# Performance work log

Measured on AMD Instinct MI355X. Metric: run time of the kernel, lower is better.

The kernel has to match this reference:

```python
import jax, jax.numpy as jnp
import numpy as np

EMBED_DIM = 1024
HEAD_SIZE = 256
B, T = 8, 2048


def setup_inputs() -> dict:
    key = jax.random.key(0)
    kx, kq, kk, kv = jax.random.split(key, 4)
    x = jax.random.normal(kx, (B, T, EMBED_DIM), dtype=jnp.float32)
    # torch Linear(E, H, bias=False): weight [H, E], y = x @ W.T; store as [E, H]
    s = 1.0 / np.sqrt(EMBED_DIM)
    Wq = jax.random.uniform(kq, (EMBED_DIM, HEAD_SIZE), jnp.float32, -s, s)
    Wk = jax.random.uniform(kk, (EMBED_DIM, HEAD_SIZE), jnp.float32, -s, s)
    Wv = jax.random.uniform(kv, (EMBED_DIM, HEAD_SIZE), jnp.float32, -s, s)
    return {"x": x, "Wq": Wq, "Wk": Wk, "Wv": Wv}


def reference(x, Wq, Wk, Wv):
    # x: [B, T, E]
    q = jnp.einsum("bte,eh->bth", x, Wq)
    k = jnp.einsum("bte,eh->bth", x, Wk)
    v = jnp.einsum("bte,eh->bth", x, Wv)
    scale = HEAD_SIZE ** -0.5
    scores = jnp.einsum("bth,bsh->bts", q, k) * scale  # [B, T, T]
    t = x.shape[1]
    causal = jnp.tril(jnp.ones((t, t), dtype=bool))
    scores = jnp.where(causal, scores, -jnp.inf)
    attn = jax.nn.softmax(scores, axis=-1)  # dropout p=0.0 -> identity
    return jnp.einsum("bts,bsh->bth", attn, v)
```

## Files before the change

kernel.cpp:

```cpp
#include <hip/hip_runtime.h>
#include <stdint.h>

#define EMBED 1024
#define HEAD  256
#define BATCH 8
#define SEQ   2048
#define NTOK  (BATCH*SEQ)

typedef __attribute__((ext_vector_type(8)))  short  s16x8;
typedef __attribute__((ext_vector_type(4)))  float  f32x4;
typedef __attribute__((ext_vector_type(16))) float  f32x16;
typedef __attribute__((ext_vector_type(4)))  unsigned short u16x4;

__device__ __forceinline__ unsigned short f2bf(float f) {
  union { float f; uint32_t u; } v; v.f = f;
  return (unsigned short)((v.u + 0x7FFFu + ((v.u >> 16) & 1u)) >> 16);
}

__device__ __forceinline__ uint32_t cvtpk(float a, float b) {
  uint32_t r;
  asm("v_cvt_pk_bf16_f32 %0, %1, %2" : "=v"(r) : "v"(a), "v"(b));
  return r;
}

__device__ __forceinline__ void gload_lds16(const void* g, void* l) {
  __builtin_amdgcn_global_load_lds((const __attribute__((address_space(1))) void*)g,
                                   (__attribute__((address_space(3))) void*)l, 16, 0, 0);
}

__global__ __launch_bounds__(256) void wt_kernel(const float* __restrict__ Wq,
                                                 const float* __restrict__ Wk,
                                                 const float* __restrict__ Wv,
                                                 unsigned short* __restrict__ Wt) {
  int idx = blockIdx.x * 256 + threadIdx.x;
  int e  = idx & (EMBED - 1);
  int hw = idx >> 10;
  int w  = hw >> 8;
  int h  = hw & 255;
  const float* W = (w == 0) ? Wq : (w == 1) ? Wk : Wv;
  float sc = (w == 0) ? 0.0625f : 1.0f;
  Wt[idx] = f2bf(W[(size_t)e * HEAD + h] * sc);
}

__global__ __launch_bounds__(256) void xprep_kernel(const float* __restrict__ x,
                                                    unsigned short* __restrict__ xb) {
  size_t i8 = ((size_t)blockIdx.x * 256 + threadIdx.x) * 8;
  f32x4 f0 = *(const f32x4*)(x + i8);
  f32x4 f1 = *(const f32x4*)(x + i8 + 4);
  u16x4 p0, p1;
  #pragma unroll
  for (int j = 0; j < 4; j++) { p0[j] = f2bf(f0[j]); p1[j] = f2bf(f1[j]); }
  *(u16x4*)(xb + i8)     = p0;
  *(u16x4*)(xb + i8 + 4) = p1;
}

__global__ __launch_bounds__(256) void proj_kernel(const unsigned short* __restrict__ xb,
    const unsigned short* __restrict__ Wt,
    unsigned short* __restrict__ qo, unsigned short* __restrict__ ko,
    unsigned short* __restrict__ vfrag) {
  __shared__ unsigned short Al[128 * 64];
  __shared__ unsigned short Bl[128 * 64];
  const int tid  = threadIdx.x;
  const int lane = tid & 63;
  const int wid  = tid >> 6;
  const int wm = wid >> 1, wn = wid & 1;
  const int bid  = blockIdx.x;
  const int xcd  = bid & 7;
  const int i6   = bid >> 3;
  const int mloc = i6 & 15;
  const int nz   = i6 >> 4;
  const int m0 = (xcd * 16 + mloc) * 128;
  const int n0 = (nz & 1) * 128;
  const int w  = nz >> 1;
  const unsigned short* Wtw = Wt + (size_t)w * 256 * EMBED;

  f32x4 acc[4][4] = {};

  for (int k0 = 0; k0 < EMBED; k0 += 64) {
    #pragma unroll
    for (int i = 0; i < 4; i++) {
      int u = tid + 256 * i;
      int row = u >> 3, sc = u & 7;
      int scs = sc ^ (row & 7);
      gload_lds16(xb + (size_t)(m0 + row) * EMBED + k0 + scs * 8,
                  &Al[i * 2048 + wid * 512]);
    }
    #pragma unroll
    for (int i = 0; i < 4; i++) {
      int u = tid + 256 * i;
      int row = u >> 3, sc = u & 7;
      int scs = sc ^ (row & 7);
      gload_lds16(Wtw + (size_t)(n0 + row) * EMBED + k0 + scs * 8,
                  &Bl[i * 2048 + wid * 512]);
    }
    __syncthreads();
    #pragma unroll
    for (int kk = 0; kk < 2; kk++) {
      s16x8 a[4], bfr[4];
      #pragma unroll
      for (int mi = 0; mi < 4; mi++) {
        int row = wm * 64 + mi * 16 + (lane & 15);
        int c = (4 * kk + (lane >> 4)) ^ (row & 7);
        a[mi] = *(const s16x8*)(&Al[row * 64 + c * 8]);
      }
      #pragma unroll
      for (int ni = 0; ni < 4; ni++) {
        int row = wn * 64 + ni * 16 + (lane & 15);
        int c = (4 * kk + (lane >> 4)) ^ (row & 7);
        bfr[ni] = *(const s16x8*)(&Bl[row * 64 + c * 8]);
      }
      #pragma unroll
      for (int mi = 0; mi < 4; mi++)
        #pragma unroll
        for (int ni = 0; ni < 4; ni++)
          acc[mi][ni] = __builtin_amdgcn_mfma_f32_16x16x32_bf16(a[mi], bfr[ni], acc[mi][ni], 0, 0, 0);
    }
    __syncthreads();
  }

  if (w < 2) {
    unsigned short* dst = (w == 0) ? qo : ko;
    #pragma unroll
    for (int mi = 0; mi < 4; mi++)
      #pragma unroll
      for (int r = 0; r < 4; r++) {
        int mrow = m0 + wm * 64 + mi * 16 + 4 * (lane >> 4) + r;
        #pragma unroll
        for (int ni = 0; ni < 4; ni++) {
          int col = n0 + wn * 64 + ni * 16 + (lane & 15);
          dst[(size_t)mrow * HEAD + col] = f2bf(acc[mi][ni][r]);
        }
      }
  } else {
    #pragma unroll
    for (int mi = 0; mi < 4; mi++) {
      int base = m0 + wm * 64 + mi * 16 + 4 * (lane >> 4);
      int toko = base & 31;
      size_t vb0 = (size_t)(base >> 11) * 524288
                 + (size_t)((base & 2047) >> 5) * 8192
                 + ((toko >> 4) & 1) * 512 + ((toko >> 3) & 1) * 256 + (toko & 7);
      #pragma unroll
      for (int ni = 0; ni < 4; ni++) {
        int col = n0 + wn * 64 + ni * 16 + (lane & 15);
        u16x4 pk;
        #pragma unroll
        for (int r = 0; r < 4; r++) pk[r] = f2bf(acc[mi][ni][r]);
        *(u16x4*)(vfrag + vb0 + (size_t)(col >> 5) * 1024 + (col & 31) * 8) = pk;
      }
    }
  }
}

__global__ __launch_bounds__(256, 1) void attn_kernel(const unsigned short* __restrict__ qb,
    const unsigned short* __restrict__ kb, const unsigned short* __restrict__ vfrag,
    float* __restrict__ out) {
  __shared__ unsigned short Kl[4][32 * 256];
  __shared__ float mls[4][2][32];
  const int tid  = threadIdx.x;
  const int lane = tid & 63;
  const int w    = tid >> 6;
  const int hi   = lane >> 5;
  const int q    = lane & 31;
  const int bid  = blockIdx.x;
  const int b = bid & 7;
  const int t = 63 - (bid >> 3);
  const unsigned short* qB = qb + (size_t)b * SEQ * HEAD;
  const unsigned short* kB = kb + (size_t)b * SEQ * HEAD;
  const unsigned short* vfB = vfrag + (size_t)b * 524288;
  float* outB = out + (size_t)b * SEQ * HEAD;
  const int qg = t * 32 + q;

  s16x8 qf[16];
  #pragma unroll
  for (int s = 0; s < 16; s++)
    qf[s] = *(const s16x8*)(qB + (size_t)qg * HEAD + s * 16 + hi * 8);

  f32x16 o[8] = {};
  float m = -1e30f, lsum = 0.f;

  const int nt = t + 1;
  const int cl = (nt + 3) >> 2;
  const int j0 = w * cl;
  const int j1 = (j0 + cl < nt) ? (j0 + cl) : nt;
  unsigned short* Kw = (unsigned short*)Kl[w];

  for (int j = j0; j < j1; j++) {
    #pragma unroll
    for (int i = 0; i < 16; i++) {
      int cl_ = i * 64 + lane;
      int key = cl_ >> 5, c = cl_ & 31;
      gload_lds16(kB + (size_t)(j * 32 + key) * HEAD + (size_t)((c ^ (key & 15)) * 8),
                  &Kw[i * 512]);
    }
    asm volatile("s_waitcnt vmcnt(0)" ::: "memory");
    __builtin_amdgcn_sched_barrier(0);
    f32x16 s0 = {}, s1 = {};
    #pragma unroll
    for (int s = 0; s < 8; s++) {
      s16x8 kf = *(const s16x8*)((const char*)Kw +
                   (q * 512 + (((2 * s + hi) ^ (q & 15)) << 4)));
      s0 = __builtin_amdgcn_mfma_f32_32x32x16_bf16(kf, qf[s], s0, 0, 0, 0);
    }
    #pragma unroll
    for (int s = 8; s < 16; s++) {
      s16x8 kf = *(const s16x8*)((const char*)Kw +
                   (q * 512 + (((2 * s + hi) ^ (q & 15)) << 4)));
      s1 = __builtin_amdgcn_mfma_f32_32x32x16_bf16(kf, qf[s], s1, 0, 0, 0);
    }
    f32x16 sv;
    #pragma unroll
    for (int r = 0; r < 16; r++) sv[r] = s0[r] + s1[r];
    if (j == t) {
      #pragma unroll
      for (int r = 0; r < 16; r++) {
        int kg = j * 32 + (r & 3) + 8 * (r >> 2) + 4 * hi;
        sv[r] = (kg > qg) ? -1e30f : sv[r];
      }
    }
    float mt = sv[0];
    #pragma unroll
    for (int r = 1; r < 16; r++) mt = fmaxf(mt, sv[r]);
    mt = fmaxf(mt, __shfl_xor(mt, 32));
    float mn = fmaxf(m, mt);
    if (!__all(mt - m <= 8.0f)) {
      float al = __expf(m - mn);
      lsum *= al;
      #pragma unroll
      for (int ht = 0; ht < 8; ht++)
        #pragma unroll
        for (int r = 0; r < 16; r++) o[ht][r] *= al;
      m = mn;
    }
    #pragma unroll
    for (int r = 0; r < 16; r++) sv[r] = __expf(sv[r] - m);
    float rs = 0.f;
    #pragma unroll
    for (int r = 0; r < 16; r++) rs += sv[r];
    rs += __shfl_xor(rs, 32);
    lsum += rs;
    uint32_t cc[8], dd[8];
    #pragma unroll
    for (int i = 0; i < 8; i++) cc[i] = cvtpk(sv[2 * i], sv[2 * i + 1]);
    #pragma unroll
    for (int i = 0; i < 8; i++) dd[i] = (uint32_t)__shfl_xor((int)cc[i], 32);
    union { s16x8 v; uint32_t u[4]; } pf0, pf1;
    pf0.u[0] = hi ? dd[2] : cc[0];
    pf0.u[1] = hi ? dd[3] : cc[1];
    pf0.u[2] = hi ? cc[2] : dd[0];
    pf0.u[3] = hi ? cc[3] : dd[1];
    pf1.u[0] = hi ? dd[6] : cc[4];
    pf1.u[1] = hi ? dd[7] : cc[5];
    pf1.u[2] = hi ? cc[6] : dd[4];
    pf1.u[3] = hi ? cc[7] : dd[5];
    const unsigned short* vT = vfB + (size_t)j * 8192 + hi * 256 + q * 8;
    #pragma unroll
    for (int ht = 0; ht < 8; ht++) {
      s16x8 vf0 = *(const s16x8*)(vT + ht * 1024);
      o[ht] = __builtin_amdgcn_mfma_f32_32x32x16_bf16(vf0, pf0.v, o[ht], 0, 0, 0);
      s16x8 vf1 = *(const s16x8*)(vT + ht * 1024 + 512);
      o[ht] = __builtin_amdgcn_mfma_f32_32x32x16_bf16(vf1, pf1.v, o[ht], 0, 0, 0);
    }
  }

  __syncthreads();
  if (lane < 32) { mls[w][0][q] = m; mls[w][1][q] = lsum; }
  __syncthreads();
  float mx = mls[0][0][q];
  #pragma unroll
  for (int w2 = 1; w2 < 4; w2++) mx = fmaxf(mx, mls[w2][0][q]);
  float L = 0.f;
  #pragma unroll
  for (int w2 = 0; w2 < 4; w2++)
    L += __expf(mls[w2][0][q] - mx) * mls[w2][1][q];
  float aown = __expf(m - mx);
  #pragma unroll
  for (int ht = 0; ht < 8; ht++)
    #pragma unroll
    for (int r = 0; r < 16; r++) o[ht][r] *= aown;

  float* obuf = (float*)&Kl[0][0];
  for (int ph = 3; ph >= 0; ph--) {
    if (w == ph) {
      #pragma unroll
      for (int ht = 0; ht < 8; ht++)
        #pragma unroll
        for (int g2 = 0; g2 < 4; g2++) {
          int gp = 8 * ht + 2 * g2 + hi;
          float* ptr = &obuf[q * 256 + ((gp ^ (q & 15)) << 2)];
          f32x4 v4 = { o[ht][4*g2], o[ht][4*g2+1], o[ht][4*g2+2], o[ht][4*g2+3] };
          if (ph != 3) { f32x4 prev = *(f32x4*)ptr;
            #pragma unroll
            for (int z = 0; z < 4; z++) v4[z] += prev[z]; }
          if (ph != 0) { *(f32x4*)ptr = v4; }
          else {
            #pragma unroll
            for (int z = 0; z < 4; z++) v4[z] /= L;
            *(f32x4*)(outB + (size_t)qg * HEAD + ht * 32 + g2 * 8 + hi * 4) = v4;
          }
        }
    }
    __syncthreads();
  }
}

extern "C" void kernel_launch(void* const* d_in, const int* in_sizes, int n_in,
                              void* d_out, int out_size, void* d_ws, size_t ws_size,
                              hipStream_t stream) {
  const float* x  = (const float*)d_in[0];
  const float* Wq = (const float*)d_in[1];
  const float* Wk = (const float*)d_in[2];
  const float* Wv = (const float*)d_in[3];
  float* out = (float*)d_out;

  unsigned short* ws = (unsigned short*)d_ws;
  unsigned short* qb    = ws;
  unsigned short* kb    = qb + (size_t)NTOK * HEAD;
  unsigned short* vfrag = kb + (size_t)NTOK * HEAD;
  unsigned short* Wt    = vfrag + (size_t)NTOK * HEAD;
  unsigned short* xb    = Wt + (size_t)3 * HEAD * EMBED;

  hipLaunchKernelGGL(wt_kernel, dim3(3 * 256 * EMBED / 256), dim3(256), 0, stream,
                     Wq, Wk, Wv, Wt);
  hipLaunchKernelGGL(xprep_kernel, dim3(NTOK * EMBED / (256 * 8)), dim3(256), 0, stream,
                     x, xb);
  hipLaunchKernelGGL(proj_kernel, dim3(768), dim3(256), 0, stream,
                     xb, Wt, qb, kb, vfrag);
  hipLaunchKernelGGL(attn_kernel, dim3(512), dim3(256), 0, stream,
                     qb, kb, vfrag, out);
}
```

Before: 133.7 us.

## Double-buffer K tiles, pair causal query tiles per block, use exp2 softmax

Each attention block now handles two query tiles, a long one and a short one (t = 63-p and t = p). This balances causal work across 256 blocks instead of 512 uneven ones. K tiles are double-buffered in LDS, so the global-to-LDS load for the next tile overlaps compute on the current one. Softmax moves to exp2 by folding log2(e) into the Q weight scale, which removes a multiply per exponent. The cost is twice the LDS per block and more serialized work per block; 256 blocks may underfill the GPU's CUs.

Result: slower. 136.4 us (+2.0%).

```diff
diff --git a/kernel.cpp b/kernel.cpp
--- a/kernel.cpp
+++ b/kernel.cpp
@@ -38,7 +38,7 @@
   int w  = hw >> 8;
   int h  = hw & 255;
   const float* W = (w == 0) ? Wq : (w == 1) ? Wk : Wv;
-  float sc = (w == 0) ? 0.0625f : 1.0f;
+  float sc = (w == 0) ? 0.09016844f : 1.0f;
   Wt[idx] = f2bf(W[(size_t)e * HEAD + h] * sc);
 }
 
@@ -154,7 +154,7 @@
 __global__ __launch_bounds__(256, 1) void attn_kernel(const unsigned short* __restrict__ qb,
     const unsigned short* __restrict__ kb, const unsigned short* __restrict__ vfrag,
     float* __restrict__ out) {
-  __shared__ unsigned short Kl[4][32 * 256];
+  __shared__ unsigned short Kl[4][2][32 * 256];
   __shared__ float mls[4][2][32];
   const int tid  = threadIdx.x;
   const int lane = tid & 63;
@@ -163,144 +163,161 @@
   const int q    = lane & 31;
   const int bid  = blockIdx.x;
   const int b = bid & 7;
-  const int t = 63 - (bid >> 3);
+  const int p = bid >> 3;
   const unsigned short* qB = qb + (size_t)b * SEQ * HEAD;
   const unsigned short* kB = kb + (size_t)b * SEQ * HEAD;
   const unsigned short* vfB = vfrag + (size_t)b * 524288;
   float* outB = out + (size_t)b * SEQ * HEAD;
-  const int qg = t * 32 + q;
-
-  s16x8 qf[16];
-  #pragma unroll
-  for (int s = 0; s < 16; s++)
-    qf[s] = *(const s16x8*)(qB + (size_t)qg * HEAD + s * 16 + hi * 8);
-
-  f32x16 o[8] = {};
-  float m = -1e30f, lsum = 0.f;
-
-  const int nt = t + 1;
-  const int cl = (nt + 3) >> 2;
-  const int j0 = w * cl;
-  const int j1 = (j0 + cl < nt) ? (j0 + cl) : nt;
   unsigned short* Kw = (unsigned short*)Kl[w];
 
-  for (int j = j0; j < j1; j++) {
-    #pragma unroll
-    for (int i = 0; i < 16; i++) {
-      int cl_ = i * 64 + lane;
-      int key = cl_ >> 5, c = cl_ & 31;
-      gload_lds16(kB + (size_t)(j * 32 + key) * HEAD + (size_t)((c ^ (key & 15)) * 8),
-                  &Kw[i * 512]);
-    }
-    asm volatile("s_waitcnt vmcnt(0)" ::: "memory");
-    __builtin_amdgcn_sched_barrier(0);
-    f32x16 s0 = {}, s1 = {};
-    #pragma unroll
-    for (int s = 0; s < 8; s++) {
-      s16x8 kf = *(const s16x8*)((const char*)Kw +
-                   (q * 512 + (((2 * s + hi) ^ (q & 15)) << 4)));
-      s0 = __builtin_amdgcn_mfma_f32_32x32x16_bf16(kf, qf[s], s0, 0, 0, 0);
-    }
-    #pragma unroll
-    for (int s = 8; s < 16; s++) {
-      s16x8 kf = *(const s16x8*)((const char*)Kw +
-                   (q * 512 + (((2 * s + hi) ^ (q & 15)) << 4)));
-      s1 = __builtin_amdgcn_mfma_f32_32x32x16_bf16(kf, qf[s], s1, 0, 0, 0);
-    }
-    f32x16 sv;
-    #pragma unroll
-    for (int r = 0; r < 16; r++) sv[r] = s0[r] + s1[r];
-    if (j == t) {
-      #pragma unroll
-      for (int r = 0; r < 16; r++) {
-        int kg = j * 32 + (r & 3) + 8 * (r >> 2) + 4 * hi;
-        sv[r] = (kg > qg) ? -1e30f : sv[r];
-      }
-    }
-    float mt = sv[0];
-    #pragma unroll
-    for (int r = 1; r < 16; r++) mt = fmaxf(mt, sv[r]);
-    mt = fmaxf(mt, __shfl_xor(mt, 32));
-    float mn = fmaxf(m, mt);
-    if (!__all(mt - m <= 8.0f)) {
-      float al = __expf(m - mn);
-      lsum *= al;
-      #pragma unroll
-      for (int ht = 0; ht < 8; ht++)
-        #pragma unroll
-        for (int r = 0; r < 16; r++) o[ht][r] *= al;
-      m = mn;
-    }
-    #pragma unroll
-    for (int r = 0; r < 16; r++) sv[r] = __expf(sv[r] - m);
-    float rs = 0.f;
-    #pragma unroll
-    for (int r = 0; r < 16; r++) rs += sv[r];
-    rs += __shfl_xor(rs, 32);
-    lsum += rs;
-    uint32_t cc[8], dd[8];
-    #pragma unroll
-    for (int i = 0; i < 8; i++) cc[i] = cvtpk(sv[2 * i], sv[2 * i + 1]);
-    #pragma unroll
-    for (int i = 0; i < 8; i++) dd[i] = (uint32_t)__shfl_xor((int)cc[i], 32);
-    union { s16x8 v; uint32_t u[4]; } pf0, pf1;
-    pf0.u[0] = hi ? dd[2] : cc[0];
-    pf0.u[1] = hi ? dd[3] : cc[1];
-    pf0.u[2] = hi ? cc[2] : dd[0];
-    pf0.u[3] = hi ? cc[3] : dd[1];
-    pf1.u[0] = hi ? dd[6] : cc[4];
-    pf1.u[1] = hi ? dd[7] : cc[5];
-    pf1.u[2] = hi ? cc[6] : dd[4];
-    pf1.u[3] = hi ? cc[7] : dd[5];
-    const unsigned short* vT = vfB + (size_t)j * 8192 + hi * 256 + q * 8;
-    #pragma unroll
-    for (int ht = 0; ht < 8; ht++) {
-      s16x8 vf0 = *(const s16x8*)(vT + ht * 1024);
-      o[ht] = __builtin_amdgcn_mfma_f32_32x32x16_bf16(vf0, pf0.v, o[ht], 0, 0, 0);
-      s16x8 vf1 = *(const s16x8*)(vT + ht * 1024 + 512);
-      o[ht] = __builtin_amdgcn_mfma_f32_32x32x16_bf16(vf1, pf1.v, o[ht], 0, 0, 0);
+  #define STAGE_K(buf, jj)                                                    \
+    _Pragma("unroll")                                                         \
+    for (int i = 0; i < 16; i++) {                                            \
+      int cl_ = i * 64 + lane;                                                \
+      int key = cl_ >> 5, c = cl_ & 31;                                       \
+      gload_lds16(kB + (size_t)((jj) * 32 + key) * HEAD + (size_t)((c ^ (key & 15)) * 8), \
+                  &Kw[(buf) * 8192 + i * 512]);                               \
+    }
+
+  for (int sl = 0; sl < 2; sl++) {
+    const int t  = sl ? p : (63 - p);
+    const int qg = t * 32 + q;
+
+    s16x8 qf[16];
+    #pragma unroll
+    for (int s = 0; s < 16; s++)
+      qf[s] = *(const s16x8*)(qB + (size_t)qg * HEAD + s * 16 + hi * 8);
+
+    f32x16 o[8] = {};
+    float m = -1e30f, lsum = 0.f;
+
+    const int nt = t + 1;
+    const int cl = (nt + 3) >> 2;
+    const int j0 = w * cl;
+    const int j1 = (j0 + cl < nt) ? (j0 + cl) : nt;
+
+    if (j0 < j1) { STAGE_K(0, j0) }
+
+    for (int j = j0; j < j1; j++) {
+      const int cur = (j - j0) & 1;
+      if (j + 1 < j1) {
+        STAGE_K(cur ^ 1, j + 1)
+        __builtin_amdgcn_sched_barrier(0);
+        asm volatile("s_waitcnt vmcnt(16)" ::: "memory");
+        __builtin_amdgcn_sched_barrier(0);
+      } else {
+        __builtin_amdgcn_sched_barrier(0);
+        asm volatile("s_waitcnt vmcnt(0)" ::: "memory");
+        __builtin_amdgcn_sched_barrier(0);
+      }
+      const char* Kc = (const char*)Kw + cur * 16384;
+      f32x16 s0 = {}, s1 = {};
+      #pragma unroll
+      for (int s = 0; s < 8; s++) {
+        s16x8 kf = *(const s16x8*)(Kc + (q * 512 + (((2 * s + hi) ^ (q & 15)) << 4)));
+        s0 = __builtin_amdgcn_mfma_f32_32x32x16_bf16(kf, qf[s], s0, 0, 0, 0);
+      }
+      #pragma unroll
+      for (int s = 8; s < 16; s++) {
+        s16x8 kf = *(const s16x8*)(Kc + (q * 512 + (((2 * s + hi) ^ (q & 15)) << 4)));
+        s1 = __builtin_amdgcn_mfma_f32_32x32x16_bf16(kf, qf[s], s1, 0, 0, 0);
+      }
+      f32x16 sv;
+      #pragma unroll
+      for (int r = 0; r < 16; r++) sv[r] = s0[r] + s1[r];
+      if (j == t) {
+        #pragma unroll
+        for (int r = 0; r < 16; r++) {
+          int kg = j * 32 + (r & 3) + 8 * (r >> 2) + 4 * hi;
+          sv[r] = (kg > qg) ? -1e30f : sv[r];
+        }
+      }
+      float mt = sv[0];
+      #pragma unroll
+      for (int r = 1; r < 16; r++) mt = fmaxf(mt, sv[r]);
+      mt = fmaxf(mt, __shfl_xor(mt, 32));
+      float mn = fmaxf(m, mt);
+      if (!__all(mt - m <= 11.5416f)) {
+        float al = exp2f(m - mn);
+        lsum *= al;
+        #pragma unroll
+        for (int ht = 0; ht < 8; ht++)
+          #pragma unroll
+          for (int r = 0; r < 16; r++) o[ht][r] *= al;
+        m = mn;
+      }
+      #pragma unroll
+      for (int r = 0; r < 16; r++) sv[r] = exp2f(sv[r] - m);
+      float rs = 0.f;
+      #pragma unroll
+      for (int r = 0; r < 16; r++) rs += sv[r];
+      rs += __shfl_xor(rs, 32);
+      lsum += rs;
+      uint32_t cc[8], dd[8];
+      #pragma unroll
+      for (int i = 0; i < 8; i++) cc[i] = cvtpk(sv[2 * i], sv[2 * i + 1]);
+      #pragma unroll
+      for (int i = 0; i < 8; i++) dd[i] = (uint32_t)__shfl_xor((int)cc[i], 32);
+      union { s16x8 v; uint32_t u[4]; } pf0, pf1;
+      pf0.u[0] = hi ? dd[2] : cc[0];
+      pf0.u[1] = hi ? dd[3] : cc[1];
+      pf0.u[2] = hi ? cc[2] : dd[0];
+      pf0.u[3] = hi ? cc[3] : dd[1];
+      pf1.u[0] = hi ? dd[6] : cc[4];
+      pf1.u[1] = hi ? dd[7] : cc[5];
+      pf1.u[2] = hi ? cc[6] : dd[4];
+      pf1.u[3] = hi ? cc[7] : dd[5];
+      const unsigned short* vT = vfB + (size_t)j * 8192 + hi * 256 + q * 8;
+      #pragma unroll
+      for (int ht = 0; ht < 8; ht++) {
+        s16x8 vf0 = *(const s16x8*)(vT + ht * 1024);
+        o[ht] = __builtin_amdgcn_mfma_f32_32x32x16_bf16(vf0, pf0.v, o[ht], 0, 0, 0);
+        s16x8 vf1 = *(const s16x8*)(vT + ht * 1024 + 512);
+        o[ht] = __builtin_amdgcn_mfma_f32_32x32x16_bf16(vf1, pf1.v, o[ht], 0, 0, 0);
+      }
+    }
+
+    __syncthreads();
+    if (lane < 32) { mls[w][0][q] = m; mls[w][1][q] = lsum; }
+    __syncthreads();
+    float mx = mls[0][0][q];
+    #pragma unroll
+    for (int w2 = 1; w2 < 4; w2++) mx = fmaxf(mx, mls[w2][0][q]);
+    float L = 0.f;
+    #pragma unroll
+    for (int w2 = 0; w2 < 4; w2++)
+      L += exp2f(mls[w2][0][q] - mx) * mls[w2][1][q];
+    float aown = exp2f(m - mx);
+    #pragma unroll
+    for (int ht = 0; ht < 8; ht++)
+      #pragma unroll
+      for (int r = 0; r < 16; r++) o[ht][r] *= aown;
+
+    float* obuf = (float*)&Kl[0][0][0];
+    for (int ph = 3; ph >= 0; ph--) {
+      if (w == ph) {
+        #pragma unroll
+        for (int ht = 0; ht < 8; ht++)
+          #pragma unroll
+          for (int g2 = 0; g2 < 4; g2++) {
+            int gp = 8 * ht + 2 * g2 + hi;
+            float* ptr = &obuf[q * 256 + ((gp ^ (q & 15)) << 2)];
+            f32x4 v4 = { o[ht][4*g2], o[ht][4*g2+1], o[ht][4*g2+2], o[ht][4*g2+3] };
+            if (ph != 3) { f32x4 prev = *(f32x4*)ptr;
+              #pragma unroll
+              for (int z = 0; z < 4; z++) v4[z] += prev[z]; }
+            if (ph != 0) { *(f32x4*)ptr = v4; }
+            else {
+              #pragma unroll
+              for (int z = 0; z < 4; z++) v4[z] /= L;
+              *(f32x4*)(outB + (size_t)qg * HEAD + ht * 32 + g2 * 8 + hi * 4) = v4;
+            }
+          }
+      }
+      __syncthreads();
     }
   }
-
-  __syncthreads();
-  if (lane < 32) { mls[w][0][q] = m; mls[w][1][q] = lsum; }
-  __syncthreads();
-  float mx = mls[0][0][q];
-  #pragma unroll
-  for (int w2 = 1; w2 < 4; w2++) mx = fmaxf(mx, mls[w2][0][q]);
-  float L = 0.f;
-  #pragma unroll
-  for (int w2 = 0; w2 < 4; w2++)
-    L += __expf(mls[w2][0][q] - mx) * mls[w2][1][q];
-  float aown = __expf(m - mx);
-  #pragma unroll
-  for (int ht = 0; ht < 8; ht++)
-    #pragma unroll
-    for (int r = 0; r < 16; r++) o[ht][r] *= aown;
-
-  float* obuf = (float*)&Kl[0][0];
-  for (int ph = 3; ph >= 0; ph--) {
-    if (w == ph) {
-      #pragma unroll
-      for (int ht = 0; ht < 8; ht++)
-        #pragma unroll
-        for (int g2 = 0; g2 < 4; g2++) {
-          int gp = 8 * ht + 2 * g2 + hi;
-          float* ptr = &obuf[q * 256 + ((gp ^ (q & 15)) << 2)];
-          f32x4 v4 = { o[ht][4*g2], o[ht][4*g2+1], o[ht][4*g2+2], o[ht][4*g2+3] };
-          if (ph != 3) { f32x4 prev = *(f32x4*)ptr;
-            #pragma unroll
-            for (int z = 0; z < 4; z++) v4[z] += prev[z]; }
-          if (ph != 0) { *(f32x4*)ptr = v4; }
-          else {
-            #pragma unroll
-            for (int z = 0; z < 4; z++) v4[z] /= L;
-            *(f32x4*)(outB + (size_t)qg * HEAD + ht * 32 + g2 * 8 + hi * 4) = v4;
-          }
-        }
-    }
-    __syncthreads();
-  }
+  #undef STAGE_K
 }
 
 extern "C" void kernel_launch(void* const* d_in, const int* in_sizes, int n_in,
@@ -325,6 +342,6 @@
                      x, xb);
   hipLaunchKernelGGL(proj_kernel, dim3(768), dim3(256), 0, stream,
                      xb, Wt, qb, kb, vfrag);
-  hipLaunchKernelGGL(attn_kernel, dim3(512), dim3(256), 0, stream,
+  hipLaunchKernelGGL(attn_kernel, dim3(256), dim3(256), 0, stream,
                      qb, kb, vfrag, out);
 }
```
